# Kernel tuning notes

Measured on AMD Instinct MI355X. Metric: run time of the kernel, lower is better.

Reference implementation:

```python
import jax, jax.numpy as jnp
import numpy as np

B, T, C = 8, 4096, 1024


def setup_inputs() -> dict:
    key = jax.random.key(0)
    ks = jax.random.split(key, 5)
    scales = (jnp.arange(C, dtype=jnp.float32) / C).reshape(1, 1, C)
    return {
        "x": jax.random.normal(ks[0], (B, T, C), dtype=jnp.float32),
        "time_decay": scales,
        "time_first": scales,
        "time_mix_k": scales,
        "time_mix_v": scales,
        "time_mix_r": scales,
        "Wk": jax.random.normal(ks[1], (C, C), dtype=jnp.float32) / np.sqrt(C),
        "Wv": jax.random.normal(ks[2], (C, C), dtype=jnp.float32) / np.sqrt(C),
        "Wr": jax.random.normal(ks[3], (C, C), dtype=jnp.float32) / np.sqrt(C),
        "Wo": jax.random.normal(ks[4], (C, C), dtype=jnp.float32) / np.sqrt(C),
    }


def _wkv(w_decay, u_first, k, v):
    # w_decay, u_first: [C]; k, v: [B, T, C]
    w = -jnp.exp(w_decay)  # per original: w = -w.exp()
    u = u_first
    kt = jnp.transpose(k, (1, 0, 2))  # [T, B, C]
    vt = jnp.transpose(v, (1, 0, 2))
    a0 = jnp.zeros((k.shape[0], k.shape[2]), dtype=k.dtype)
    b0 = jnp.zeros_like(a0)
    p0 = jnp.full_like(a0, -1e38)  # running max exponent

    def step(carry, kv):
        a, b, p = carry
        k_t, v_t = kv
        # output at t (includes bonus u for current token)
        q = jnp.maximum(p, u + k_t)
        e1 = jnp.exp(p - q)
        e2 = jnp.exp(u + k_t - q)
        y = (e1 * a + e2 * v_t) / (e1 * b + e2)
        # state update with decay w
        q2 = jnp.maximum(p + w, k_t)
        f1 = jnp.exp(p + w - q2)
        f2 = jnp.exp(k_t - q2)
        return (f1 * a + f2 * v_t, f1 * b + f2, q2), y

    _, y = jax.lax.scan(step, (a0, b0, p0), (kt, vt))
    return jnp.transpose(y, (1, 0, 2))  # [B, T, C]


def reference(x, time_decay, time_first, time_mix_k, time_mix_v, time_mix_r, Wk, Wv, Wr, Wo):
    # time shift: prev token, zero-padded at t=0 (ZeroPad2d((0,0,1,-1)))
    x_prev = jnp.pad(x, ((0, 0), (1, 0), (0, 0)))[:, :-1]
    # torch.lerp(a, b, w) = a + w*(b-a)
    xk = x_prev + time_mix_k * (x - x_prev)
    xv = x_prev + time_mix_v * (x - x_prev)
    xr = x_prev + time_mix_r * (x - x_prev)
    k = jnp.einsum('btc,dc->btd', xk, Wk)
    v = jnp.einsum('btc,dc->btd', xv, Wv)
    sr = jax.nn.sigmoid(jnp.einsum('btc,dc->btd', xr, Wr))
    wkv = _wkv(time_decay.reshape(-1), time_first.reshape(-1), k, v)
    return jnp.einsum('btc,dc->btd', sr * wkv, Wo)
```

## Files before the change

kernel.cpp:

```cpp
#include <hip/hip_runtime.h>
#include <hip/hip_bf16.h>
#include <hip/hip_fp16.h>


#define BH 8
#define TT 4096
#define CC 1024
#define NCH 64
#define CHL (TT / NCH)

typedef _Float16       f16x8  __attribute__((ext_vector_type(8)));
typedef float          f32x4  __attribute__((ext_vector_type(4)));
typedef unsigned short ushort_t;

__device__ __forceinline__ ushort_t f2h_u(float f) {
  return __half_as_ushort(__float2half(f));
}

#define GLOAD_LDS16(g, l)                                                     \
  __builtin_amdgcn_global_load_lds(                                           \
      (const __attribute__((address_space(1))) unsigned int*)(g),             \
      (__attribute__((address_space(3))) unsigned int*)(l), 16, 0, 0)

#define BARRIER() do { asm volatile("" ::: "memory");                        \
                       __builtin_amdgcn_s_barrier();                          \
                       asm volatile("" ::: "memory"); } while (0)

#define LGKM0() do { asm volatile("s_waitcnt lgkmcnt(0)" ::: "memory");      \
                     __builtin_amdgcn_sched_barrier(0); } while (0)

#define WAITV(n) do { asm volatile("s_waitcnt vmcnt(" #n ")" ::: "memory");  \
                      __builtin_amdgcn_sched_barrier(0); } while (0)

__global__ __launch_bounds__(256)
void split_w(const float* __restrict__ W0, const float* __restrict__ W1,
             const float* __restrict__ W2, const float* __restrict__ W3,
             ushort_t* __restrict__ out)
{
  int idx = blockIdx.x * 256 + threadIdx.x;
  int w = idx >> 20;
  int e = idx & (CC * CC - 1);
  const float* src = (w == 0) ? W0 : (w == 1) ? W1 : (w == 2) ? W2 : W3;
  out[(size_t)w * CC * CC + e] = f2h_u(src[e]);
}

__global__ __launch_bounds__(256)
void lerp3(const float* __restrict__ x,
           const float* __restrict__ mk, const float* __restrict__ mv,
           const float* __restrict__ mr,
           ushort_t* __restrict__ xk, ushort_t* __restrict__ xv,
           ushort_t* __restrict__ xr)
{
  const int idx = blockIdx.x * 256 + threadIdx.x;
  const int m = idx >> 8;
  const int c = (idx & 255) * 4;
  const size_t e = (size_t)m * CC + c;
  float4 cu = *(const float4*)(x + e);
  float4 pv = make_float4(0.f, 0.f, 0.f, 0.f);
  if ((m & (TT - 1)) != 0) pv = *(const float4*)(x + e - CC);

  const float* mixes[3] = {mk, mv, mr};
  ushort_t* outs[3] = {xk, xv, xr};
  #pragma unroll
  for (int z = 0; z < 3; ++z) {
    float4 mx = *(const float4*)(mixes[z] + c);
    float a0 = pv.x + mx.x * (cu.x - pv.x);
    float a1 = pv.y + mx.y * (cu.y - pv.y);
    float a2 = pv.z + mx.z * (cu.z - pv.z);
    float a3 = pv.w + mx.w * (cu.w - pv.w);
    *(ushort4*)(outs[z] + e) = make_ushort4(f2h_u(a0), f2h_u(a1), f2h_u(a2), f2h_u(a3));
  }
}

template<int EPI>
__global__ __launch_bounds__(512, 2)
void gemm_f16(const ushort_t* __restrict__ Ab, const ushort_t* __restrict__ Bb,
              void* __restrict__ Dv)
{
  constexpr int NS = 16;
  const size_t nbt = (size_t)BH * TT * CC;

  __shared__ __align__(16) ushort_t lds[2][4][8192];

  const int tid  = threadIdx.x;
  const int wave = tid >> 6, lane = tid & 63;
  const int wm = wave & 1, wn = wave >> 1;
  const int lr = lane & 15, kg = lane >> 4;

  const int z = blockIdx.z;
  const ushort_t* Ah = Ab + (size_t)z * nbt;
  const ushort_t* Bh = Bb + (size_t)z * CC * CC;

  const int bid = blockIdx.x;
  const int swz = (bid & 7) * 64 + (bid >> 3);
  const int m0 = (swz >> 2) * 256;
  const int n0 = (swz & 3) * 256;

  f32x4 acc[8][4] = {};

  auto stage = [&](int s, int part) {
    if (s >= NS) return;
    const int kk = s * 64 + (part >> 1) * 32;
    const ushort_t* g0 = (part & 1) ? Bh : Ah;
    const int r0 = (part & 1) ? n0 : m0;
    #pragma unroll
    for (int c = 0; c < 2; ++c) {
      const int row = c * 128 + (tid >> 2);
      const int q   = (tid & 3) ^ ((row >> 1) & 3);
      const ushort_t* src = g0 + (size_t)(r0 + row) * CC + kk + q * 8;
      ushort_t* dst = &lds[s & 1][part][c * 4096 + wave * 512];
      GLOAD_LDS16(src, dst);
    }
  };
  auto rdA = [&](int b, int ks, int fm) -> f16x8 {
    const int row = wm * 128 + fm * 16 + lr;
    const int q   = kg ^ ((row >> 1) & 3);
    return *(const f16x8*)&lds[b][ks * 2][row * 32 + q * 8];
  };
  auto rdB = [&](int b, int ks, int fn) -> f16x8 {
    const int row = wn * 64 + fn * 16 + lr;
    const int q   = kg ^ ((row >> 1) & 3);
    return *(const f16x8*)&lds[b][ks * 2 + 1][row * 32 + q * 8];
  };

  stage(0, 0); stage(0, 1); stage(0, 2); stage(0, 3);
  stage(1, 0); stage(1, 1);
  WAITV(8);
  BARRIER();

  for (int s = 0; s < NS; ++s) {
    const int b = s & 1;
    f16x8 bfr[4], afr[4];

    #pragma unroll
    for (int fn = 0; fn < 4; ++fn) bfr[fn] = rdB(b, 0, fn);
    #pragma unroll
    for (int i = 0; i < 4; ++i) afr[i] = rdA(b, 0, i);
    stage(s + 1, 2);
    BARRIER();
    LGKM0();
    __builtin_amdgcn_s_setprio(1);
    #pragma unroll
    for (int i = 0; i < 4; ++i)
      #pragma unroll
      for (int fn = 0; fn < 4; ++fn)
        acc[i][fn] = __builtin_amdgcn_mfma_f32_16x16x32_f16(afr[i], bfr[fn], acc[i][fn], 0, 0, 0);
    __builtin_amdgcn_s_setprio(0);
    BARRIER();

    #pragma unroll
    for (int i = 0; i < 4; ++i) afr[i] = rdA(b, 0, 4 + i);
    stage(s + 1, 3);
    BARRIER();
    LGKM0();
    __builtin_amdgcn_s_setprio(1);
    #pragma unroll
    for (int i = 0; i < 4; ++i)
      #pragma unroll
      for (int fn = 0; fn < 4; ++fn)
        acc[4 + i][fn] = __builtin_amdgcn_mfma_f32_16x16x32_f16(afr[i], bfr[fn], acc[4 + i][fn], 0, 0, 0);
    __builtin_amdgcn_s_setprio(0);
    if (s < NS - 1) { WAITV(8); } else { WAITV(0); }
    BARRIER();

    #pragma unroll
    for (int fn = 0; fn < 4; ++fn) bfr[fn] = rdB(b, 1, fn);
    #pragma unroll
    for (int i = 0; i < 4; ++i) afr[i] = rdA(b, 1, i);
    stage(s + 2, 0);
    BARRIER();
    LGKM0();
    __builtin_amdgcn_s_setprio(1);
    #pragma unroll
    for (int i = 0; i < 4; ++i)
      #pragma unroll
      for (int fn = 0; fn < 4; ++fn)
        acc[i][fn] = __builtin_amdgcn_mfma_f32_16x16x32_f16(afr[i], bfr[fn], acc[i][fn], 0, 0, 0);
    __builtin_amdgcn_s_setprio(0);
    BARRIER();

    #pragma unroll
    for (int i = 0; i < 4; ++i) afr[i] = rdA(b, 1, 4 + i);
    stage(s + 2, 1);
    BARRIER();
    LGKM0();
    __builtin_amdgcn_s_setprio(1);
    #pragma unroll
    for (int i = 0; i < 4; ++i)
      #pragma unroll
      for (int fn = 0; fn < 4; ++fn)
        acc[4 + i][fn] = __builtin_amdgcn_mfma_f32_16x16x32_f16(afr[i], bfr[fn], acc[4 + i][fn], 0, 0, 0);
    __builtin_amdgcn_s_setprio(0);
    if (s < NS - 2)       { WAITV(8); }
    else if (s == NS - 2) { WAITV(4); }
    BARRIER();
  }

  if (EPI == 0) {
    float* Df = (float*)Dv;
    #pragma unroll
    for (int fm = 0; fm < 8; ++fm)
      #pragma unroll
      for (int fn = 0; fn < 4; ++fn) {
        const int col  = n0 + wn * 64 + fn * 16 + lr;
        const int rowb = m0 + wm * 128 + fm * 16 + kg * 4;
        #pragma unroll
        for (int r = 0; r < 4; ++r)
          Df[(size_t)(rowb + r) * CC + col] = acc[fm][fn][r];
      }
  } else {
    __half* Dh = (__half*)Dv + (size_t)z * nbt;
    __half* ep = (__half*)&lds[0][0][0];
    const int rowl = tid >> 4;
    const int ck   = tid & 15;
    #pragma unroll
    for (int s = 0; s < 8; ++s) {
      __syncthreads();
      #pragma unroll
      for (int fn = 0; fn < 4; ++fn)
        #pragma unroll
        for (int r = 0; r < 4; ++r)
          ep[(wm * 16 + kg * 4 + r) * 280 + wn * 64 + fn * 16 + lr] =
              __float2half(acc[s][fn][r]);
      __syncthreads();
      uint4 v0 = *(const uint4*)&ep[rowl * 280 + ck * 16];
      uint4 v1 = *(const uint4*)&ep[rowl * 280 + ck * 16 + 8];
      const int grow = m0 + (rowl >> 4) * 128 + s * 16 + (rowl & 15);
      __half* dst = Dh + (size_t)grow * CC + n0 + ck * 16;
      *(uint4*)dst = v0;
      *(uint4*)(dst + 8) = v1;
    }
  }
}

__global__ __launch_bounds__(256)
void wkv_phase_a(const __half* __restrict__ kb, const __half* __restrict__ vb,
                 const float* __restrict__ decay,
                 float* __restrict__ SA, float* __restrict__ SB, float* __restrict__ SP)
{
  const int idx = blockIdx.x * 256 + threadIdx.x;
  const int c  = idx & (CC - 1);
  const int bc = idx >> 10;
  const int ch = bc & (NCH - 1);
  const int b  = bc >> 6;
  const float w = -__expf(decay[c]);
  float aa = 0.f, bb = 0.f, pp = -1e38f;
  size_t base = ((size_t)b * TT + (size_t)ch * CHL) * CC + c;
  #pragma unroll 4
  for (int t = 0; t < CHL; ++t) {
    const float kt = __half2float(kb[base]);
    const float vt = __half2float(vb[base]);
    const float q2 = fmaxf(pp + w, kt);
    const float f1 = __expf(pp + w - q2);
    const float f2 = __expf(kt - q2);
    aa = f1 * aa + f2 * vt; bb = f1 * bb + f2; pp = q2;
    base += CC;
  }
  SA[idx] = aa; SB[idx] = bb; SP[idx] = pp;
}

__global__ __launch_bounds__(256)
void wkv_combine(float* __restrict__ SA, float* __restrict__ SB, float* __restrict__ SP,
                 const float* __restrict__ decay)
{
  const int idx = blockIdx.x * 256 + threadIdx.x;
  const int c = idx & (CC - 1);
  const int b = idx >> 10;
  const float w  = -__expf(decay[c]);
  const float wL = w * (float)CHL;
  float aa = 0.f, bb = 0.f, pp = -1e38f;
  for (int ch = 0; ch < NCH; ++ch) {
    const size_t s = ((size_t)b * NCH + ch) * CC + c;
    const float la = SA[s], lb = SB[s], lp = SP[s];
    SA[s] = aa; SB[s] = bb; SP[s] = pp;
    const float pw = pp + wL;
    const float q  = fmaxf(pw, lp);
    const float e1 = __expf(pw - q);
    const float e2 = __expf(lp - q);
    aa = e1 * aa + e2 * la; bb = e1 * bb + e2 * lb; pp = q;
  }
}

__global__ __launch_bounds__(256)
void wkv_phase_c(const __half* __restrict__ kb, const __half* __restrict__ vb,
                 const __half* __restrict__ rb, const float* __restrict__ decay,
                 const float* __restrict__ first,
                 const float* __restrict__ SA, const float* __restrict__ SB,
                 const float* __restrict__ SP,
                 ushort_t* __restrict__ yh)
{
  const int idx = blockIdx.x * 256 + threadIdx.x;
  const int c  = idx & (CC - 1);
  const int bc = idx >> 10;
  const int ch = bc & (NCH - 1);
  const int b  = bc >> 6;
  const float w = -__expf(decay[c]);
  const float u = first[c];
  float aa = SA[idx], bb = SB[idx], pp = SP[idx];
  size_t base = ((size_t)b * TT + (size_t)ch * CHL) * CC + c;
  #pragma unroll 4
  for (int t = 0; t < CHL; ++t) {
    const float kt = __half2float(kb[base]);
    const float vt = __half2float(vb[base]);
    const float rt = __half2float(rb[base]);
    const float q  = fmaxf(pp, u + kt);
    const float e1 = __expf(pp - q);
    const float e2 = __expf(u + kt - q);
    const float yv = (e1 * aa + e2 * vt) / (e1 * bb + e2);
    const float sr = 1.f / (1.f + __expf(-rt));
    yh[base] = f2h_u(sr * yv);
    const float q2 = fmaxf(pp + w, kt);
    const float f1 = __expf(pp + w - q2);
    const float f2 = __expf(kt - q2);
    aa = f1 * aa + f2 * vt; bb = f1 * bb + f2; pp = q2;
    base += CC;
  }
}

extern "C" void kernel_launch(void* const* d_in, const int* in_sizes, int n_in,
                              void* d_out, int out_size, void* d_ws, size_t ws_size,
                              hipStream_t stream) {
  const float* x     = (const float*)d_in[0];
  const float* decay = (const float*)d_in[1];
  const float* first = (const float*)d_in[2];
  const float* mk    = (const float*)d_in[3];
  const float* mv    = (const float*)d_in[4];
  const float* mr    = (const float*)d_in[5];
  const float* Wk    = (const float*)d_in[6];
  const float* Wv    = (const float*)d_in[7];
  const float* Wr    = (const float*)d_in[8];
  const float* Wo    = (const float*)d_in[9];
  float* out = (float*)d_out;

  const size_t nbt = (size_t)BH * TT * CC;
  const size_t WS  = (size_t)CC * CC;
  char* p = (char*)d_ws;
  ushort_t* xk   = (ushort_t*)(p);
  ushort_t* xv   = (ushort_t*)(p +  67108864);
  ushort_t* xr   = (ushort_t*)(p + 134217728);
  __half*   kbuf = (__half*)  (p + 201326592);
  __half*   vbuf = (__half*)  (p + 268435456);
  __half*   rbuf = (__half*)  (p + 335544320);
  ushort_t* Wsp  = (ushort_t*)(p + 402653184);
  float*    SA   = (float*)   (p + 411041792);
  float*    SB   = (float*)   (p + 413138944);
  float*    SP   = (float*)   (p + 415236096);

  dim3 blk(256);
  const dim3 gblk(512);
  const unsigned lerpg = (unsigned)(nbt / 4 / 256);

  split_w<<<dim3(4 * CC * CC / 256), blk, 0, stream>>>(Wk, Wv, Wr, Wo, Wsp);
  lerp3<<<dim3(lerpg), blk, 0, stream>>>(x, mk, mv, mr, xk, xv, xr);

  gemm_f16<1><<<dim3(512, 1, 3), gblk, 0, stream>>>(xk, Wsp, (void*)kbuf);

  const int nscan = BH * NCH * CC;
  wkv_phase_a<<<dim3(nscan / 256), blk, 0, stream>>>(kbuf, vbuf, decay, SA, SB, SP);
  wkv_combine<<<dim3(BH * CC / 256), blk, 0, stream>>>(SA, SB, SP, decay);
  wkv_phase_c<<<dim3(nscan / 256), blk, 0, stream>>>(kbuf, vbuf, rbuf, decay, first,
                                                     SA, SB, SP, xk);

  gemm_f16<0><<<dim3(512, 1, 1), gblk, 0, stream>>>(xk, Wsp + 3 * WS, (void*)out);
}
```

Baseline: 492.6 us.

## Fuse K/V/R projection GEMMs into one persistent-pipeline kernel per tile

```diff
diff --git a/kernel.cpp b/kernel.cpp
--- a/kernel.cpp
+++ b/kernel.cpp
@@ -72,24 +72,172 @@
   }
 }
 
-template<int EPI>
 __global__ __launch_bounds__(512, 2)
-void gemm_f16(const ushort_t* __restrict__ Ab, const ushort_t* __restrict__ Bb,
-              void* __restrict__ Dv)
-{
-  constexpr int NS = 16;
+void gemm_fused3(const ushort_t* __restrict__ Ab, const ushort_t* __restrict__ Bb,
+                 __half* __restrict__ Db)
+{
+  constexpr int NS = 48;
   const size_t nbt = (size_t)BH * TT * CC;
 
   __shared__ __align__(16) ushort_t lds[2][4][8192];
+  __shared__ __align__(16) __half   ep2[32 * 280];
 
   const int tid  = threadIdx.x;
   const int wave = tid >> 6, lane = tid & 63;
   const int wm = wave & 1, wn = wave >> 1;
   const int lr = lane & 15, kg = lane >> 4;
 
-  const int z = blockIdx.z;
-  const ushort_t* Ah = Ab + (size_t)z * nbt;
-  const ushort_t* Bh = Bb + (size_t)z * CC * CC;
+  const int bid = blockIdx.x;
+  const int swz = (bid & 7) * 64 + (bid >> 3);
+  const int m0 = (swz >> 2) * 256;
+  const int n0 = (swz & 3) * 256;
+
+  f32x4 acc[8][4] = {};
+
+  auto stage = [&](int u, int part) {
+    if (u >= NS) return;
+    const int comp = u >> 4;
+    const int kk = (u & 15) * 64 + (part >> 1) * 32;
+    const ushort_t* g0 = (part & 1) ? (Bb + (size_t)comp * CC * CC)
+                                    : (Ab + (size_t)comp * nbt);
+    const int r0 = (part & 1) ? n0 : m0;
+    #pragma unroll
+    for (int c = 0; c < 2; ++c) {
+      const int row = c * 128 + (tid >> 2);
+      const int q   = (tid & 3) ^ ((row >> 1) & 3);
+      const ushort_t* src = g0 + (size_t)(r0 + row) * CC + kk + q * 8;
+      ushort_t* dst = &lds[u & 1][part][c * 4096 + wave * 512];
+      GLOAD_LDS16(src, dst);
+    }
+  };
+  auto rdA = [&](int b, int ks, int fm) -> f16x8 {
+    const int row = wm * 128 + fm * 16 + lr;
+    const int q   = kg ^ ((row >> 1) & 3);
+    return *(const f16x8*)&lds[b][ks * 2][row * 32 + q * 8];
+  };
+  auto rdB = [&](int b, int ks, int fn) -> f16x8 {
+    const int row = wn * 64 + fn * 16 + lr;
+    const int q   = kg ^ ((row >> 1) & 3);
+    return *(const f16x8*)&lds[b][ks * 2 + 1][row * 32 + q * 8];
+  };
+
+  stage(0, 0); stage(0, 1); stage(0, 2); stage(0, 3);
+  stage(1, 0); stage(1, 1);
+  WAITV(8);
+  BARRIER();
+
+  #pragma unroll 1
+  for (int u = 0; u < NS; ++u) {
+    const int b = u & 1;
+    f16x8 bfr[4], afr[4];
+
+    #pragma unroll
+    for (int fn = 0; fn < 4; ++fn) bfr[fn] = rdB(b, 0, fn);
+    #pragma unroll
+    for (int i = 0; i < 4; ++i) afr[i] = rdA(b, 0, i);
+    stage(u + 1, 2);
+    BARRIER();
+    LGKM0();
+    __builtin_amdgcn_s_setprio(1);
+    #pragma unroll
+    for (int i = 0; i < 4; ++i)
+      #pragma unroll
+      for (int fn = 0; fn < 4; ++fn)
+        acc[i][fn] = __builtin_amdgcn_mfma_f32_16x16x32_f16(afr[i], bfr[fn], acc[i][fn], 0, 0, 0);
+    __builtin_amdgcn_s_setprio(0);
+    BARRIER();
+
+    #pragma unroll
+    for (int i = 0; i < 4; ++i) afr[i] = rdA(b, 0, 4 + i);
+    stage(u + 1, 3);
+    BARRIER();
+    LGKM0();
+    __builtin_amdgcn_s_setprio(1);
+    #pragma unroll
+    for (int i = 0; i < 4; ++i)
+      #pragma unroll
+      for (int fn = 0; fn < 4; ++fn)
+        acc[4 + i][fn] = __builtin_amdgcn_mfma_f32_16x16x32_f16(afr[i], bfr[fn], acc[4 + i][fn], 0, 0, 0);
+    __builtin_amdgcn_s_setprio(0);
+    if (u < NS - 1) { WAITV(8); } else { WAITV(0); }
+    BARRIER();
+
+    #pragma unroll
+    for (int fn = 0; fn < 4; ++fn) bfr[fn] = rdB(b, 1, fn);
+    #pragma unroll
+    for (int i = 0; i < 4; ++i) afr[i] = rdA(b, 1, i);
+    stage(u + 2, 0);
+    BARRIER();
+    LGKM0();
+    __builtin_amdgcn_s_setprio(1);
+    #pragma unroll
+    for (int i = 0; i < 4; ++i)
+      #pragma unroll
+      for (int fn = 0; fn < 4; ++fn)
+        acc[i][fn] = __builtin_amdgcn_mfma_f32_16x16x32_f16(afr[i], bfr[fn], acc[i][fn], 0, 0, 0);
+    __builtin_amdgcn_s_setprio(0);
+    BARRIER();
+
+    #pragma unroll
+    for (int i = 0; i < 4; ++i) afr[i] = rdA(b, 1, 4 + i);
+    stage(u + 2, 1);
+    BARRIER();
+    LGKM0();
+    __builtin_amdgcn_s_setprio(1);
+    #pragma unroll
+    for (int i = 0; i < 4; ++i)
+      #pragma unroll
+      for (int fn = 0; fn < 4; ++fn)
+        acc[4 + i][fn] = __builtin_amdgcn_mfma_f32_16x16x32_f16(afr[i], bfr[fn], acc[4 + i][fn], 0, 0, 0);
+    __builtin_amdgcn_s_setprio(0);
+    if (u < NS - 2)       { WAITV(8); }
+    else if (u == NS - 2) { WAITV(4); }
+    BARRIER();
+
+    if ((u & 15) == 15) {
+      __half* Dh = Db + (size_t)(u >> 4) * nbt;
+      const int rowl = tid >> 4;
+      const int ck   = tid & 15;
+      #pragma unroll
+      for (int sl = 0; sl < 8; ++sl) {
+        LGKM0();
+        BARRIER();
+        #pragma unroll
+        for (int fn = 0; fn < 4; ++fn)
+          #pragma unroll
+          for (int r = 0; r < 4; ++r)
+            ep2[(wm * 16 + kg * 4 + r) * 280 + wn * 64 + fn * 16 + lr] =
+                __float2half(acc[sl][fn][r]);
+        LGKM0();
+        BARRIER();
+        uint4 v0 = *(const uint4*)&ep2[rowl * 280 + ck * 16];
+        uint4 v1 = *(const uint4*)&ep2[rowl * 280 + ck * 16 + 8];
+        const int grow = m0 + (rowl >> 4) * 128 + sl * 16 + (rowl & 15);
+        __half* dst = Dh + (size_t)grow * CC + n0 + ck * 16;
+        *(uint4*)dst = v0;
+        *(uint4*)(dst + 8) = v1;
+      }
+      #pragma unroll
+      for (int fm = 0; fm < 8; ++fm)
+        #pragma unroll
+        for (int fn = 0; fn < 4; ++fn)
+          acc[fm][fn] = (f32x4){0.f, 0.f, 0.f, 0.f};
+    }
+  }
+}
+
+__global__ __launch_bounds__(512, 2)
+void gemm_out(const ushort_t* __restrict__ Ah, const ushort_t* __restrict__ Bh,
+              float* __restrict__ Df)
+{
+  constexpr int NS = 16;
+
+  __shared__ __align__(16) ushort_t lds[2][4][8192];
+
+  const int tid  = threadIdx.x;
+  const int wave = tid >> 6, lane = tid & 63;
+  const int wm = wave & 1, wn = wave >> 1;
+  const int lr = lane & 15, kg = lane >> 4;
 
   const int bid = blockIdx.x;
   const int swz = (bid & 7) * 64 + (bid >> 3);
@@ -196,41 +344,16 @@
     BARRIER();
   }
 
-  if (EPI == 0) {
-    float* Df = (float*)Dv;
-    #pragma unroll
-    for (int fm = 0; fm < 8; ++fm)
-      #pragma unroll
-      for (int fn = 0; fn < 4; ++fn) {
-        const int col  = n0 + wn * 64 + fn * 16 + lr;
-        const int rowb = m0 + wm * 128 + fm * 16 + kg * 4;
-        #pragma unroll
-        for (int r = 0; r < 4; ++r)
-          Df[(size_t)(rowb + r) * CC + col] = acc[fm][fn][r];
-      }
-  } else {
-    __half* Dh = (__half*)Dv + (size_t)z * nbt;
-    __half* ep = (__half*)&lds[0][0][0];
-    const int rowl = tid >> 4;
-    const int ck   = tid & 15;
-    #pragma unroll
-    for (int s = 0; s < 8; ++s) {
-      __syncthreads();
-      #pragma unroll
-      for (int fn = 0; fn < 4; ++fn)
-        #pragma unroll
-        for (int r = 0; r < 4; ++r)
-          ep[(wm * 16 + kg * 4 + r) * 280 + wn * 64 + fn * 16 + lr] =
-              __float2half(acc[s][fn][r]);
-      __syncthreads();
-      uint4 v0 = *(const uint4*)&ep[rowl * 280 + ck * 16];
-      uint4 v1 = *(const uint4*)&ep[rowl * 280 + ck * 16 + 8];
-      const int grow = m0 + (rowl >> 4) * 128 + s * 16 + (rowl & 15);
-      __half* dst = Dh + (size_t)grow * CC + n0 + ck * 16;
-      *(uint4*)dst = v0;
-      *(uint4*)(dst + 8) = v1;
+  #pragma unroll
+  for (int fm = 0; fm < 8; ++fm)
+    #pragma unroll
+    for (int fn = 0; fn < 4; ++fn) {
+      const int col  = n0 + wn * 64 + fn * 16 + lr;
+      const int rowb = m0 + wm * 128 + fm * 16 + kg * 4;
+      #pragma unroll
+      for (int r = 0; r < 4; ++r)
+        Df[(size_t)(rowb + r) * CC + col] = acc[fm][fn][r];
     }
-  }
 }
 
 __global__ __launch_bounds__(256)
@@ -353,7 +476,7 @@
   split_w<<<dim3(4 * CC * CC / 256), blk, 0, stream>>>(Wk, Wv, Wr, Wo, Wsp);
   lerp3<<<dim3(lerpg), blk, 0, stream>>>(x, mk, mv, mr, xk, xv, xr);
 
-  gemm_f16<1><<<dim3(512, 1, 3), gblk, 0, stream>>>(xk, Wsp, (void*)kbuf);
+  gemm_fused3<<<dim3(512), gblk, 0, stream>>>(xk, Wsp, kbuf);
 
   const int nscan = BH * NCH * CC;
   wkv_phase_a<<<dim3(nscan / 256), blk, 0, stream>>>(kbuf, vbuf, decay, SA, SB, SP);
@@ -361,5 +484,5 @@
   wkv_phase_c<<<dim3(nscan / 256), blk, 0, stream>>>(kbuf, vbuf, rbuf, decay, first,
                                                      SA, SB, SP, xk);
 
-  gemm_f16<0><<<dim3(512, 1, 1), gblk, 0, stream>>>(xk, Wsp + 3 * WS, (void*)out);
-}
+  gemm_out<<<dim3(512), gblk, 0, stream>>>(xk, Wsp + 3 * WS, out);
+}
```

After: 508.7 us. +3.3%, slower.
